# Kernel optimization log

Hardware: AMD Instinct MI355X
Metric: run time of the kernel (lower is better)

The kernel has to match this reference:

```python
import jax, jax.numpy as jnp
import numpy as np

B, S, D, H = 4, 1024, 1024, 16
DK = D // H


def setup_inputs() -> dict:
    key = jax.random.key(0)
    ks = jax.random.split(key, 14)
    scale = 1.0 / np.sqrt(D)
    inp = {
        "Qx": jax.random.normal(ks[0], (B, S, D), jnp.float32),
        "Kx": jax.random.normal(ks[1], (B, S, D), jnp.float32),
        "Vx": jax.random.normal(ks[2], (B, S, D), jnp.float32),
        "prob_phn": jax.random.uniform(ks[3], (B, S, S), jnp.float32),
        "mask": jax.random.randint(ks[4], (B, S, S), 0, 2, jnp.int32),
        "lambda_val": 1,
        "Wq": jax.random.normal(ks[5], (D, D), jnp.float32) * scale,
        "bq": jnp.zeros((D,), jnp.float32),
        "Wk": jax.random.normal(ks[6], (D, D), jnp.float32) * scale,
        "bk": jnp.zeros((D,), jnp.float32),
        "Wv": jax.random.normal(ks[7], (D, D), jnp.float32) * scale,
        "bv": jnp.zeros((D,), jnp.float32),
        "Wo": jax.random.normal(ks[8], (D, D), jnp.float32) * scale,
        "bo": jnp.zeros((D,), jnp.float32),
    }
    return inp


def _split_heads(x):
    # [B,S,D] -> [B,H,S,DK]
    b, s, _ = x.shape
    return x.reshape(b, s, H, DK).transpose(0, 2, 1, 3)


def reference(Qx, Kx, Vx, prob_phn, mask, lambda_val, Wq, bq, Wk, bk, Wv, bv, Wo, bo):
    q = _split_heads(Qx @ Wq.T + bq)
    k = _split_heads(Kx @ Wk.T + bk)
    v = _split_heads(Vx @ Wv.T + bv)
    scores = jnp.einsum("bhqd,bhkd->bhqk", q, k) / jnp.sqrt(jnp.float32(DK))
    if lambda_val > 0:
        # prob_phn: [B,S,S] -> transpose last two dims, broadcast over heads
        scores = scores - lambda_val * jnp.swapaxes(prob_phn, -2, -1)[:, None]
    scores = jnp.where(mask[:, None] == 0, jnp.float32(-1e9), scores)
    probs = jax.nn.softmax(scores, axis=-1)
    attn = jnp.einsum("bhqk,bhkd->bhqd", probs, v)
    out = attn.transpose(0, 2, 1, 3).reshape(Qx.shape[0], Qx.shape[1], D)
    out = out @ Wo.T + bo
    return (out, mask)
```

## Files before the change

kernel.cpp:

```cpp
#include <hip/hip_runtime.h>
#include <hip/hip_bf16.h>
#include <cstdint>
#include <cstddef>

#define BB 4
#define SS 1024
#define DD 1024
#define HH 16
#define DKK 64

typedef unsigned short u16;
typedef __bf16 bf16_t;
typedef __attribute__((ext_vector_type(8))) bf16_t bf16x8;
typedef __attribute__((ext_vector_type(4))) float floatx4;

static __device__ inline u16 f2bf(float f) {
    union { float f; unsigned u; } v; v.f = f;
    unsigned r = v.u + 0x7fffu + ((v.u >> 16) & 1u);
    return (u16)(r >> 16);
}

static __device__ inline void load16_lds(const void* g, void* l) {
    __builtin_amdgcn_global_load_lds(
        (const __attribute__((address_space(1))) unsigned int*)g,
        (__attribute__((address_space(3))) unsigned int*)l,
        16, 0, 0);
}

static __device__ inline int swz64(int row, int c) { return row * 64 + ((c ^ (row & 7)) * 8); }
static __device__ inline int swz32(int row, int c) { return row * 32 + ((c ^ ((row >> 1) & 3)) * 8); }

static __device__ inline float lam_val(const int* p) {
    int v = *p;
    if (v >= -100000 && v <= 100000) return (float)v;
    union { int i; float f; } u; u.i = v; return u.f;
}

__global__ void prep_kernel(const float* __restrict__ Qx, const float* __restrict__ Kx,
                            const float* __restrict__ Vx,
                            const float* __restrict__ Wq, const float* __restrict__ Wk,
                            const float* __restrict__ Wv, const float* __restrict__ Wo,
                            const float* __restrict__ prob, const int* __restrict__ mask,
                            const int* __restrict__ lam_p,
                            u16* __restrict__ Xq, u16* __restrict__ Xk, u16* __restrict__ Xv,
                            u16* __restrict__ wq, u16* __restrict__ wk,
                            u16* __restrict__ wv, u16* __restrict__ wo,
                            u16* __restrict__ biasB, float* __restrict__ maskOut)
{
    __shared__ float tile[64][65];
    const int blk = blockIdx.x, tid = threadIdx.x;

    if (blk >= 1024) {
        const int cb = blk - 1024;
        const int base = cb * 1024;
        const float* src; u16* dst; int off0;
        if (base < 3145728) {
            int s = base >> 20;  off0 = base & 1048575;
            src = (s == 0) ? Qx : (s == 1) ? Kx : Vx;
            dst = (s == 0) ? Xq : (s == 1) ? Xk : Xv;
        } else {
            int v2 = base - 3145728;
            int s = v2 >> 18;  off0 = v2 & 262143;
            src = (s == 0) ? Wq : (s == 1) ? Wk : (s == 2) ? Wv : Wo;
            dst = (s == 0) ? wq : (s == 1) ? wk : (s == 2) ? wv : wo;
        }
        float4 f[4];
        #pragma unroll
        for (int r = 0; r < 4; ++r)
            f[r] = ((const float4*)src)[off0 + r * 256 + tid];
        #pragma unroll
        for (int r = 0; r < 4; ++r) {
            ushort4 o;
            o.x = f2bf(f[r].x); o.y = f2bf(f[r].y);
            o.z = f2bf(f[r].z); o.w = f2bf(f[r].w);
            ((ushort4*)dst)[off0 + r * 256 + tid] = o;
        }
        return;
    }

    const int b = blk >> 8;
    const int q0 = ((blk >> 4) & 15) * 64, k0 = (blk & 15) * 64;
    #pragma unroll
    for (int rr = 0; rr < 4; ++rr) {
        int unit = rr * 256 + tid;
        int kl = unit >> 4, qi = unit & 15;
        float4 p4 = *(const float4*)&prob[((size_t)(b * SS + k0 + kl)) * SS + q0 + qi * 4];
        tile[kl][qi * 4 + 0] = p4.x;
        tile[kl][qi * 4 + 1] = p4.y;
        tile[kl][qi * 4 + 2] = p4.z;
        tile[kl][qi * 4 + 3] = p4.w;
    }
    __syncthreads();
    const float lam = lam_val(lam_p);
    #pragma unroll
    for (int rr = 0; rr < 4; ++rr) {
        int pair = rr * 256 + tid;
        int q = pair >> 4, k4 = pair & 15;
        size_t oidx = ((size_t)(b * SS + q0 + q)) * SS + k0 + k4 * 4;
        int4 m4 = *(const int4*)&mask[oidx];
        float p0 = tile[k4 * 4 + 0][q];
        float p1 = tile[k4 * 4 + 1][q];
        float p2 = tile[k4 * 4 + 2][q];
        float p3 = tile[k4 * 4 + 3][q];
        ushort4 bb;
        bb.x = f2bf((m4.x == 0) ? -1e9f : -lam * p0);
        bb.y = f2bf((m4.y == 0) ? -1e9f : -lam * p1);
        bb.z = f2bf((m4.z == 0) ? -1e9f : -lam * p2);
        bb.w = f2bf((m4.w == 0) ? -1e9f : -lam * p3);
        *(ushort4*)&biasB[oidx] = bb;
        if (maskOut) {
            float4 mf = { (float)m4.x, (float)m4.y, (float)m4.z, (float)m4.w };
            *(float4*)&maskOut[oidx] = mf;
        }
    }
}

template <int MODE>
static __device__ inline void gemm_body(const u16* __restrict__ A, const u16* __restrict__ W,
                                        const float* __restrict__ bias,
                                        u16* __restrict__ Cb, float* __restrict__ Cf)
{
    constexpr int K = 1024, N = 1024;
    __shared__ __align__(16) u16 As[128 * 32];
    __shared__ __align__(16) u16 Bs[128 * 32];
    const int tid = threadIdx.x;
    const int wv = tid >> 6, ln = tid & 63, l15 = ln & 15, quad = ln >> 4;
    const int mBase = blockIdx.y * 128;
    const int nBase = blockIdx.x * 128;
    const int wm = (wv & 1) * 64, wn = (wv >> 1) * 64;

    const u16* Aptr[2]; const u16* Wptr[2];
    #pragma unroll
    for (int r = 0; r < 2; ++r) {
        int p = r * 256 + wv * 64 + ln;
        int row = p >> 2;
        int c = (p & 3) ^ ((row >> 1) & 3);
        Aptr[r] = A + (size_t)(mBase + row) * K + c * 8;
        Wptr[r] = W + (size_t)(nBase + row) * K + c * 8;
    }

    floatx4 acc[4][4] = {};

    for (int k0 = 0; k0 < K; k0 += 32) {
        __syncthreads();
        #pragma unroll
        for (int r = 0; r < 2; ++r) {
            load16_lds(Aptr[r] + k0, &As[(r * 256 + wv * 64) * 8]);
            load16_lds(Wptr[r] + k0, &Bs[(r * 256 + wv * 64) * 8]);
        }
        __syncthreads();
        bf16x8 af[4], bfr[4];
        #pragma unroll
        for (int i = 0; i < 4; ++i)
            af[i] = *(const bf16x8*)&As[swz32(wm + i * 16 + l15, quad)];
        #pragma unroll
        for (int j = 0; j < 4; ++j)
            bfr[j] = *(const bf16x8*)&Bs[swz32(wn + j * 16 + l15, quad)];
        #pragma unroll
        for (int i = 0; i < 4; ++i)
            #pragma unroll
            for (int j = 0; j < 4; ++j)
                acc[i][j] = __builtin_amdgcn_mfma_f32_16x16x32_bf16(af[i], bfr[j], acc[i][j], 0, 0, 0);
    }

    #pragma unroll
    for (int i = 0; i < 4; ++i) {
        #pragma unroll
        for (int j = 0; j < 4; ++j) {
            int col = nBase + wn + j * 16 + l15;
            float bcol = bias[col];
            if (MODE == 2) {
                int hh = col >> 6, dk = col & 63;
                int row0 = mBase + wm + i * 16 + quad * 4;
                int bb = row0 >> 10, s = row0 & 1023;
                ushort4 v4;
                v4.x = f2bf(acc[i][j][0] + bcol);
                v4.y = f2bf(acc[i][j][1] + bcol);
                v4.z = f2bf(acc[i][j][2] + bcol);
                v4.w = f2bf(acc[i][j][3] + bcol);
                *(ushort4*)&Cb[((size_t)((bb * HH + hh) * DKK) + dk) * SS + s] = v4;
            } else {
                #pragma unroll
                for (int r = 0; r < 4; ++r) {
                    int row = mBase + wm + i * 16 + quad * 4 + r;
                    float v = acc[i][j][r] + bcol;
                    if (MODE == 1) Cf[(size_t)row * N + col] = v;
                    else           Cb[(size_t)row * N + col] = f2bf(v);
                }
            }
        }
    }
}

__global__ __launch_bounds__(256) void gemm_qkv_kernel(
    const u16* __restrict__ Xq, const u16* __restrict__ Xk, const u16* __restrict__ Xv,
    const u16* __restrict__ Wq, const u16* __restrict__ Wk, const u16* __restrict__ Wv,
    const float* __restrict__ bq, const float* __restrict__ bk, const float* __restrict__ bv,
    u16* __restrict__ Cq, u16* __restrict__ Ck, u16* __restrict__ Vtout)
{
    const int z = blockIdx.z;
    if (z == 2) {
        gemm_body<2>(Xv, Wv, bv, Vtout, nullptr);
    } else {
        const u16* A = (z == 0) ? Xq : Xk;
        const u16* W = (z == 0) ? Wq : Wk;
        const float* bias = (z == 0) ? bq : bk;
        u16* C = (z == 0) ? Cq : Ck;
        gemm_body<0>(A, W, bias, C, nullptr);
    }
}

__global__ __launch_bounds__(256) void gemm_out_kernel(
    const u16* __restrict__ A, const u16* __restrict__ W,
    const float* __restrict__ bias, float* __restrict__ Cf)
{
    gemm_body<1>(A, W, bias, nullptr, Cf);
}

__global__ __launch_bounds__(256) void attn_kernel(
    const u16* __restrict__ Qf, const u16* __restrict__ Kf,
    const u16* __restrict__ Vt, const u16* __restrict__ biasB,
    u16* __restrict__ Attn)
{
    __shared__ __align__(16) u16 Qs[128 * 64];
    __shared__ __align__(16) u16 Ks[2][64 * 64];
    __shared__ __align__(16) u16 Vs[2][64 * 64];
    __shared__ __align__(16) u16 Ps[4][32 * 72];
    const int tid = threadIdx.x;
    const int wv = tid >> 6, ln = tid & 63, l15 = ln & 15, quad = ln >> 4;
    const int qt = blockIdx.x, h = blockIdx.y, b = blockIdx.z;
    const int q0 = qt * 128;

    int row64[2], col64[2];
    #pragma unroll
    for (int r = 0; r < 2; ++r) {
        int p = r * 256 + wv * 64 + ln;
        row64[r] = p >> 3;
        col64[r] = ((p & 7) ^ (row64[r] & 7)) * 8;
    }

    #pragma unroll
    for (int r = 0; r < 4; ++r) {
        int p = r * 256 + wv * 64 + ln;
        int row = p >> 3;
        int c = ((p & 7) ^ (row & 7)) * 8;
        load16_lds(Qf + ((size_t)(b * SS + q0 + row)) * DD + h * DKK + c,
                   &Qs[(r * 256 + wv * 64) * 8]);
    }

    const size_t vt_head = ((size_t)(b * HH + h)) * DKK * SS;
    const u16* Kp[2]; const u16* Vp[2];
    #pragma unroll
    for (int r = 0; r < 2; ++r) {
        Kp[r] = Kf + ((size_t)(b * SS + row64[r])) * DD + h * DKK + col64[r];
        Vp[r] = Vt + vt_head + (size_t)row64[r] * SS + col64[r];
    }

    #pragma unroll
    for (int r = 0; r < 2; ++r) {
        load16_lds(Kp[r], &Ks[0][(r * 256 + wv * 64) * 8]);
        load16_lds(Vp[r], &Vs[0][(r * 256 + wv * 64) * 8]);
    }
    __syncthreads();

    bf16x8 aq[2][2];
    #pragma unroll
    for (int m = 0; m < 2; ++m)
        #pragma unroll
        for (int t = 0; t < 2; ++t)
            aq[m][t] = *(const bf16x8*)&Qs[swz64(wv * 32 + m * 16 + l15, t * 4 + quad)];

    const u16* bp[2][4];
    #pragma unroll
    for (int m = 0; m < 2; ++m)
        #pragma unroll
        for (int r = 0; r < 4; ++r)
            bp[m][r] = biasB + ((size_t)(b * SS + q0 + wv * 32 + m * 16 + quad * 4 + r)) * SS + l15;

    float bv_[2][4][4];
    #pragma unroll
    for (int m = 0; m < 2; ++m)
        #pragma unroll
        for (int j = 0; j < 4; ++j)
            #pragma unroll
            for (int r = 0; r < 4; ++r)
                bv_[m][j][r] = __uint_as_float((unsigned)bp[m][r][j * 16] << 16);

    floatx4 o[2][4] = {};
    float rsum[2][4] = {};

    for (int kt = 0; kt < 16; ++kt) {
        const int cur = kt & 1, nxt = cur ^ 1;

        if (kt < 15) {
            #pragma unroll
            for (int r = 0; r < 2; ++r) {
                Kp[r] += (size_t)64 * DD; Vp[r] += 64;
                load16_lds(Kp[r], &Ks[nxt][(r * 256 + wv * 64) * 8]);
                load16_lds(Vp[r], &Vs[nxt][(r * 256 + wv * 64) * 8]);
            }
        }

        floatx4 sfr[2][4];
        #pragma unroll
        for (int j = 0; j < 4; ++j) {
            bf16x8 bk0 = *(const bf16x8*)&Ks[cur][swz64(j * 16 + l15, quad)];
            bf16x8 bk1 = *(const bf16x8*)&Ks[cur][swz64(j * 16 + l15, 4 + quad)];
            #pragma unroll
            for (int m = 0; m < 2; ++m) {
                floatx4 s = {};
                s = __builtin_amdgcn_mfma_f32_16x16x32_bf16(aq[m][0], bk0, s, 0, 0, 0);
                sfr[m][j] = __builtin_amdgcn_mfma_f32_16x16x32_bf16(aq[m][1], bk1, s, 0, 0, 0);
            }
        }

        #pragma unroll
        for (int m = 0; m < 2; ++m)
            #pragma unroll
            for (int j = 0; j < 4; ++j)
                #pragma unroll
                for (int r = 0; r < 4; ++r) {
                    float p = __expf(fmaf(sfr[m][j][r], 0.125f, bv_[m][j][r]));
                    rsum[m][r] += p;
                    Ps[wv][(m * 16 + quad * 4 + r) * 72 + j * 16 + l15] =
                        (u16)(__float_as_uint(p) >> 16);
                }

        if (kt < 15) {
            #pragma unroll
            for (int m = 0; m < 2; ++m)
                #pragma unroll
                for (int r = 0; r < 4; ++r) {
                    bp[m][r] += 64;
                    #pragma unroll
                    for (int j = 0; j < 4; ++j)
                        bv_[m][j][r] = __uint_as_float((unsigned)bp[m][r][j * 16] << 16);
                }
        }

        #pragma unroll
        for (int t = 0; t < 2; ++t) {
            bf16x8 ap0 = *(const bf16x8*)&Ps[wv][l15 * 72 + t * 32 + quad * 8];
            bf16x8 ap1 = *(const bf16x8*)&Ps[wv][(16 + l15) * 72 + t * 32 + quad * 8];
            #pragma unroll
            for (int j = 0; j < 4; ++j) {
                bf16x8 bvv = *(const bf16x8*)&Vs[cur][swz64(j * 16 + l15, t * 4 + quad)];
                o[0][j] = __builtin_amdgcn_mfma_f32_16x16x32_bf16(ap0, bvv, o[0][j], 0, 0, 0);
                o[1][j] = __builtin_amdgcn_mfma_f32_16x16x32_bf16(ap1, bvv, o[1][j], 0, 0, 0);
            }
        }

        __syncthreads();
    }

    #pragma unroll
    for (int m = 0; m < 2; ++m)
        #pragma unroll
        for (int r = 0; r < 4; ++r) {
            float s = rsum[m][r];
            s += __shfl_xor(s, 1);
            s += __shfl_xor(s, 2);
            s += __shfl_xor(s, 4);
            s += __shfl_xor(s, 8);
            rsum[m][r] = 1.0f / s;
        }
    #pragma unroll
    for (int m = 0; m < 2; ++m)
        #pragma unroll
        for (int j = 0; j < 4; ++j)
            #pragma unroll
            for (int r = 0; r < 4; ++r) {
                int srow = q0 + wv * 32 + m * 16 + quad * 4 + r;
                int dk = j * 16 + l15;
                Attn[((size_t)(b * SS + srow)) * DD + h * DKK + dk] =
                    f2bf(o[m][j][r] * rsum[m][r]);
            }
}

extern "C" void kernel_launch(void* const* d_in, const int* in_sizes, int n_in,
                              void* d_out, int out_size, void* d_ws, size_t ws_size,
                              hipStream_t stream)
{
    const float* Qx  = (const float*)d_in[0];
    const float* Kx  = (const float*)d_in[1];
    const float* Vx  = (const float*)d_in[2];
    const float* prob = (const float*)d_in[3];
    const int*   mask = (const int*)d_in[4];
    const int*   lam  = (const int*)d_in[5];
    const float* Wq  = (const float*)d_in[6];
    const float* bq  = (const float*)d_in[7];
    const float* Wk  = (const float*)d_in[8];
    const float* bk  = (const float*)d_in[9];
    const float* Wv  = (const float*)d_in[10];
    const float* bv  = (const float*)d_in[11];
    const float* Wo  = (const float*)d_in[12];
    const float* bo  = (const float*)d_in[13];

    char* ws = (char*)d_ws;
    const size_t MB = 1024 * 1024;
    u16*   Xq     = (u16*)(ws + 0 * MB);
    u16*   Xk     = (u16*)(ws + 8 * MB);
    u16*   Xv     = (u16*)(ws + 16 * MB);
    u16*   wq     = (u16*)(ws + 24 * MB);
    u16*   wk     = (u16*)(ws + 26 * MB);
    u16*   wvp    = (u16*)(ws + 28 * MB);
    u16*   wo     = (u16*)(ws + 30 * MB);
    u16*   q_flat = (u16*)(ws + 32 * MB);
    u16*   k_flat = (u16*)(ws + 40 * MB);
    u16*   vt     = (u16*)(ws + 56 * MB);
    u16*   biasB  = (u16*)(ws + 64 * MB);
    u16*   attn   = (u16*)(ws + 80 * MB);

    float* maskOut = (out_size >= 2 * BB * SS * DD) ? (float*)d_out + (size_t)BB * SS * DD
                                                    : nullptr;

    prep_kernel<<<5120, 256, 0, stream>>>(Qx, Kx, Vx, Wq, Wk, Wv, Wo, prob, mask, lam,
                                          Xq, Xk, Xv, wq, wk, wvp, wo, biasB, maskOut);
    gemm_qkv_kernel<<<dim3(8, 32, 3), 256, 0, stream>>>(Xq, Xk, Xv, wq, wk, wvp,
                                                        bq, bk, bv, q_flat, k_flat, vt);
    attn_kernel<<<dim3(8, 16, 4), 256, 0, stream>>>(q_flat, k_flat, vt, biasB, attn);
    gemm_out_kernel<<<dim3(8, 32, 1), 256, 0, stream>>>(attn, wo, bo, (float*)d_out);
}
```

Baseline: 258.4 us.

## Shrink attention query tile to 64 rows, transpose QK MFMA, use exp2 with prescaled bias

The attention kernel now processes 64 query rows per block instead of 128 and launches twice as many blocks. It computes S^T via swapped MFMA operands so each lane reads contiguous bias entries as packed uint2 and writes packed P to LDS. Softmax uses exp2 with log2e folded into the QK scale and into the precomputed bias. The K/V double buffering is dropped in favour of single buffers with two barriers per step, which trades load/compute overlap for lower LDS use and higher occupancy. K/V reuse per block is also halved.

```diff
diff --git a/kernel.cpp b/kernel.cpp
--- a/kernel.cpp
+++ b/kernel.cpp
@@ -13,6 +13,9 @@
 typedef __bf16 bf16_t;
 typedef __attribute__((ext_vector_type(8))) bf16_t bf16x8;
 typedef __attribute__((ext_vector_type(4))) float floatx4;
+
+#define LOG2E 1.4426950408889634f
+#define QKSCALE 0.18033688011112042f
 
 static __device__ inline u16 f2bf(float f) {
     union { float f; unsigned u; } v; v.f = f;
@@ -91,7 +94,7 @@
         tile[kl][qi * 4 + 3] = p4.w;
     }
     __syncthreads();
-    const float lam = lam_val(lam_p);
+    const float lamс = lam_val(lam_p) * LOG2E;
     #pragma unroll
     for (int rr = 0; rr < 4; ++rr) {
         int pair = rr * 256 + tid;
@@ -103,10 +106,10 @@
         float p2 = tile[k4 * 4 + 2][q];
         float p3 = tile[k4 * 4 + 3][q];
         ushort4 bb;
-        bb.x = f2bf((m4.x == 0) ? -1e9f : -lam * p0);
-        bb.y = f2bf((m4.y == 0) ? -1e9f : -lam * p1);
-        bb.z = f2bf((m4.z == 0) ? -1e9f : -lam * p2);
-        bb.w = f2bf((m4.w == 0) ? -1e9f : -lam * p3);
+        bb.x = f2bf((m4.x == 0) ? -1.5e9f : -lamс * p0);
+        bb.y = f2bf((m4.y == 0) ? -1.5e9f : -lamс * p1);
+        bb.z = f2bf((m4.z == 0) ? -1.5e9f : -lamс * p2);
+        bb.w = f2bf((m4.w == 0) ? -1.5e9f : -lamс * p3);
         *(ushort4*)&biasB[oidx] = bb;
         if (maskOut) {
             float4 mf = { (float)m4.x, (float)m4.y, (float)m4.z, (float)m4.w };
@@ -222,14 +225,15 @@
     const u16* __restrict__ Vt, const u16* __restrict__ biasB,
     u16* __restrict__ Attn)
 {
-    __shared__ __align__(16) u16 Qs[128 * 64];
-    __shared__ __align__(16) u16 Ks[2][64 * 64];
-    __shared__ __align__(16) u16 Vs[2][64 * 64];
-    __shared__ __align__(16) u16 Ps[4][32 * 72];
+    __shared__ __align__(16) u16 Qs[64 * 64];
+    __shared__ __align__(16) u16 Ks[64 * 64];
+    __shared__ __align__(16) u16 Vs[64 * 64];
+    __shared__ __align__(16) u16 Ps[4][16 * 72];
+    __shared__ float Rs[4][16];
     const int tid = threadIdx.x;
     const int wv = tid >> 6, ln = tid & 63, l15 = ln & 15, quad = ln >> 4;
     const int qt = blockIdx.x, h = blockIdx.y, b = blockIdx.z;
-    const int q0 = qt * 128;
+    const int q0 = qt * 64;
 
     int row64[2], col64[2];
     #pragma unroll
@@ -240,13 +244,15 @@
     }
 
     #pragma unroll
-    for (int r = 0; r < 4; ++r) {
-        int p = r * 256 + wv * 64 + ln;
-        int row = p >> 3;
-        int c = ((p & 7) ^ (row & 7)) * 8;
-        load16_lds(Qf + ((size_t)(b * SS + q0 + row)) * DD + h * DKK + c,
+    for (int r = 0; r < 2; ++r)
+        load16_lds(Qf + ((size_t)(b * SS + q0 + row64[r])) * DD + h * DKK + col64[r],
                    &Qs[(r * 256 + wv * 64) * 8]);
-    }
+    __syncthreads();
+
+    bf16x8 aq[2];
+    #pragma unroll
+    for (int t = 0; t < 2; ++t)
+        aq[t] = *(const bf16x8*)&Qs[swz64(wv * 16 + l15, t * 4 + quad)];
 
     const size_t vt_head = ((size_t)(b * HH + h)) * DKK * SS;
     const u16* Kp[2]; const u16* Vp[2];
@@ -256,125 +262,79 @@
         Vp[r] = Vt + vt_head + (size_t)row64[r] * SS + col64[r];
     }
 
-    #pragma unroll
-    for (int r = 0; r < 2; ++r) {
-        load16_lds(Kp[r], &Ks[0][(r * 256 + wv * 64) * 8]);
-        load16_lds(Vp[r], &Vs[0][(r * 256 + wv * 64) * 8]);
-    }
-    __syncthreads();
-
-    bf16x8 aq[2][2];
-    #pragma unroll
-    for (int m = 0; m < 2; ++m)
-        #pragma unroll
-        for (int t = 0; t < 2; ++t)
-            aq[m][t] = *(const bf16x8*)&Qs[swz64(wv * 32 + m * 16 + l15, t * 4 + quad)];
-
-    const u16* bp[2][4];
-    #pragma unroll
-    for (int m = 0; m < 2; ++m)
-        #pragma unroll
-        for (int r = 0; r < 4; ++r)
-            bp[m][r] = biasB + ((size_t)(b * SS + q0 + wv * 32 + m * 16 + quad * 4 + r)) * SS + l15;
-
-    float bv_[2][4][4];
-    #pragma unroll
-    for (int m = 0; m < 2; ++m)
+    const u16* bp = biasB + ((size_t)(b * SS + q0 + wv * 16 + l15)) * SS + quad * 4;
+
+    floatx4 o[4] = {};
+    float rsum = 0.f;
+
+    for (int kt = 0; kt < 16; ++kt) {
+        const int kk0 = kt * 64;
+        __syncthreads();
+        #pragma unroll
+        for (int r = 0; r < 2; ++r) {
+            load16_lds(Kp[r] + (size_t)kk0 * DD, &Ks[(r * 256 + wv * 64) * 8]);
+            load16_lds(Vp[r] + kk0, &Vs[(r * 256 + wv * 64) * 8]);
+        }
+        __syncthreads();
+
+        uint2 braw[4];
         #pragma unroll
         for (int j = 0; j < 4; ++j)
-            #pragma unroll
-            for (int r = 0; r < 4; ++r)
-                bv_[m][j][r] = __uint_as_float((unsigned)bp[m][r][j * 16] << 16);
-
-    floatx4 o[2][4] = {};
-    float rsum[2][4] = {};
-
-    for (int kt = 0; kt < 16; ++kt) {
-        const int cur = kt & 1, nxt = cur ^ 1;
-
-        if (kt < 15) {
-            #pragma unroll
-            for (int r = 0; r < 2; ++r) {
-                Kp[r] += (size_t)64 * DD; Vp[r] += 64;
-                load16_lds(Kp[r], &Ks[nxt][(r * 256 + wv * 64) * 8]);
-                load16_lds(Vp[r], &Vs[nxt][(r * 256 + wv * 64) * 8]);
-            }
-        }
-
-        floatx4 sfr[2][4];
+            braw[j] = *(const uint2*)&bp[kk0 + j * 16];
+
+        floatx4 sfr[4];
         #pragma unroll
         for (int j = 0; j < 4; ++j) {
-            bf16x8 bk0 = *(const bf16x8*)&Ks[cur][swz64(j * 16 + l15, quad)];
-            bf16x8 bk1 = *(const bf16x8*)&Ks[cur][swz64(j * 16 + l15, 4 + quad)];
-            #pragma unroll
-            for (int m = 0; m < 2; ++m) {
-                floatx4 s = {};
-                s = __builtin_amdgcn_mfma_f32_16x16x32_bf16(aq[m][0], bk0, s, 0, 0, 0);
-                sfr[m][j] = __builtin_amdgcn_mfma_f32_16x16x32_bf16(aq[m][1], bk1, s, 0, 0, 0);
-            }
-        }
-
-        #pragma unroll
-        for (int m = 0; m < 2; ++m)
-            #pragma unroll
-            for (int j = 0; j < 4; ++j)
-                #pragma unroll
-                for (int r = 0; r < 4; ++r) {
-                    float p = __expf(fmaf(sfr[m][j][r], 0.125f, bv_[m][j][r]));
-                    rsum[m][r] += p;
-                    Ps[wv][(m * 16 + quad * 4 + r) * 72 + j * 16 + l15] =
-                        (u16)(__float_as_uint(p) >> 16);
-                }
-
-        if (kt < 15) {
-            #pragma unroll
-            for (int m = 0; m < 2; ++m)
-                #pragma unroll
-                for (int r = 0; r < 4; ++r) {
-                    bp[m][r] += 64;
-                    #pragma unroll
-                    for (int j = 0; j < 4; ++j)
-                        bv_[m][j][r] = __uint_as_float((unsigned)bp[m][r][j * 16] << 16);
-                }
+            bf16x8 bk0 = *(const bf16x8*)&Ks[swz64(j * 16 + l15, quad)];
+            bf16x8 bk1 = *(const bf16x8*)&Ks[swz64(j * 16 + l15, 4 + quad)];
+            floatx4 s = {};
+            s = __builtin_amdgcn_mfma_f32_16x16x32_bf16(bk0, aq[0], s, 0, 0, 0);
+            sfr[j] = __builtin_amdgcn_mfma_f32_16x16x32_bf16(bk1, aq[1], s, 0, 0, 0);
+        }
+
+        #pragma unroll
+        for (int j = 0; j < 4; ++j) {
+            float b0 = __uint_as_float(braw[j].x << 16);
+            float b1 = __uint_as_float(braw[j].x & 0xffff0000u);
+            float b2 = __uint_as_float(braw[j].y << 16);
+            float b3 = __uint_as_float(braw[j].y & 0xffff0000u);
+            float p0 = __builtin_amdgcn_exp2f(fmaf(sfr[j][0], QKSCALE, b0));
+            float p1 = __builtin_amdgcn_exp2f(fmaf(sfr[j][1], QKSCALE, b1));
+            float p2 = __builtin_amdgcn_exp2f(fmaf(sfr[j][2], QKSCALE, b2));
+            float p3 = __builtin_amdgcn_exp2f(fmaf(sfr[j][3], QKSCALE, b3));
+            rsum += (p0 + p1) + (p2 + p3);
+            uint2 pk;
+            pk.x = (__float_as_uint(p0) >> 16) | (__float_as_uint(p1) & 0xffff0000u);
+            pk.y = (__float_as_uint(p2) >> 16) | (__float_as_uint(p3) & 0xffff0000u);
+            *(uint2*)&Ps[wv][l15 * 72 + j * 16 + quad * 4] = pk;
         }
 
         #pragma unroll
         for (int t = 0; t < 2; ++t) {
-            bf16x8 ap0 = *(const bf16x8*)&Ps[wv][l15 * 72 + t * 32 + quad * 8];
-            bf16x8 ap1 = *(const bf16x8*)&Ps[wv][(16 + l15) * 72 + t * 32 + quad * 8];
+            bf16x8 ap = *(const bf16x8*)&Ps[wv][l15 * 72 + t * 32 + quad * 8];
             #pragma unroll
             for (int j = 0; j < 4; ++j) {
-                bf16x8 bvv = *(const bf16x8*)&Vs[cur][swz64(j * 16 + l15, t * 4 + quad)];
-                o[0][j] = __builtin_amdgcn_mfma_f32_16x16x32_bf16(ap0, bvv, o[0][j], 0, 0, 0);
-                o[1][j] = __builtin_amdgcn_mfma_f32_16x16x32_bf16(ap1, bvv, o[1][j], 0, 0, 0);
+                bf16x8 bvv = *(const bf16x8*)&Vs[swz64(j * 16 + l15, t * 4 + quad)];
+                o[j] = __builtin_amdgcn_mfma_f32_16x16x32_bf16(ap, bvv, o[j], 0, 0, 0);
             }
         }
-
-        __syncthreads();
-    }
-
-    #pragma unroll
-    for (int m = 0; m < 2; ++m)
+    }
+
+    rsum += __shfl_xor(rsum, 16);
+    rsum += __shfl_xor(rsum, 32);
+    if (ln < 16) Rs[wv][l15] = 1.0f / rsum;
+    float4 rv = *(const float4*)&Rs[wv][quad * 4];
+
+    #pragma unroll
+    for (int j = 0; j < 4; ++j) {
         #pragma unroll
         for (int r = 0; r < 4; ++r) {
-            float s = rsum[m][r];
-            s += __shfl_xor(s, 1);
-            s += __shfl_xor(s, 2);
-            s += __shfl_xor(s, 4);
-            s += __shfl_xor(s, 8);
-            rsum[m][r] = 1.0f / s;
-        }
-    #pragma unroll
-    for (int m = 0; m < 2; ++m)
-        #pragma unroll
-        for (int j = 0; j < 4; ++j)
-            #pragma unroll
-            for (int r = 0; r < 4; ++r) {
-                int srow = q0 + wv * 32 + m * 16 + quad * 4 + r;
-                int dk = j * 16 + l15;
-                Attn[((size_t)(b * SS + srow)) * DD + h * DKK + dk] =
-                    f2bf(o[m][j][r] * rsum[m][r]);
-            }
+            int srow = q0 + wv * 16 + quad * 4 + r;
+            int dk = j * 16 + l15;
+            float ri = (r == 0) ? rv.x : (r == 1) ? rv.y : (r == 2) ? rv.z : rv.w;
+            Attn[((size_t)(b * SS + srow)) * DD + h * DKK + dk] = f2bf(o[j][r] * ri);
+        }
+    }
 }
 
 extern "C" void kernel_launch(void* const* d_in, const int* in_sizes, int n_in,
@@ -418,6 +378,6 @@
                                           Xq, Xk, Xv, wq, wk, wvp, wo, biasB, maskOut);
     gemm_qkv_kernel<<<dim3(8, 32, 3), 256, 0, stream>>>(Xq, Xk, Xv, wq, wk, wvp,
                                                         bq, bk, bv, q_flat, k_flat, vt);
-    attn_kernel<<<dim3(8, 16, 4), 256, 0, stream>>>(q_flat, k_flat, vt, biasB, attn);
+    attn_kernel<<<dim3(16, 16, 4), 256, 0, stream>>>(q_flat, k_flat, vt, biasB, attn);
     gemm_out_kernel<<<dim3(8, 32, 1), 256, 0, stream>>>(attn, wo, bo, (float*)d_out);
 }
```

After: 258.0 us. Within noise of the previous version (-0.2%).
